# Kernel optimization log

Measured on AMD Instinct MI355X. Metric: run time of the kernel, lower is better.

Reference implementation:

```python
import jax, jax.numpy as jnp
import numpy as np
import math

NUM_HEADS = 16
N_WIRES = 8  # == d_k


def setup_inputs() -> dict:
    key = jax.random.key(0)
    k1, k2, k3, k4 = jax.random.split(key, 4)
    B, S, E = 4, 2048, NUM_HEADS * N_WIRES
    x = jax.random.normal(k1, (B, S, E), dtype=jnp.float32)
    theta = jax.random.normal(k2, (N_WIRES,), dtype=jnp.float32)
    W_combine = jax.random.normal(k3, (E, E), dtype=jnp.float32) * (1.0 / math.sqrt(E))
    b_combine = jax.random.normal(k4, (E,), dtype=jnp.float32) * 0.01
    return {"x": x, "theta": theta, "W_combine": W_combine, "b_combine": b_combine}


def _quantum_heads(x, theta, H, dk):
    # since single-qubit RX gates compose and the state stays a product state.
    B, S, E = x.shape
    proj = x.reshape(B, S, H, dk)  # [B,S,H,dk]
    return jnp.cos(proj + theta)   # theta broadcasts over wires (dk == n_wires)


def reference(x, theta, W_combine, b_combine):
    B, S, E = x.shape
    H, dk = NUM_HEADS, N_WIRES
    qkv = _quantum_heads(x, theta, H, dk)          # [B,S,H,dk]; q = k = v
    qh = jnp.transpose(qkv, (0, 2, 1, 3))           # [B,H,S,dk]
    scores = jnp.einsum('bhqd,bhkd->bhqk', qh, qh) / math.sqrt(dk)
    attn = jax.nn.softmax(scores, axis=-1)          # [B,H,S,S]
    out = jnp.einsum('bhqk,bhkd->bhqd', attn, qh)   # [B,H,S,dk]
    out = jnp.transpose(out, (0, 2, 1, 3)).reshape(B, S, E)
    return out @ W_combine.T + b_combine
```

## Files before the change

kernel.cpp:

```cpp
#include <hip/hip_runtime.h>

typedef _Float16 f16;
typedef _Float16 f16x2 __attribute__((ext_vector_type(2)));
typedef __fp16   h16x2 __attribute__((ext_vector_type(2)));
typedef _Float16 f16x4 __attribute__((ext_vector_type(4)));
typedef float    f32x4 __attribute__((ext_vector_type(4)));
typedef unsigned int u32;
typedef unsigned int u32x2v __attribute__((ext_vector_type(2)));

#define NB 4
#define NS 2048
#define NH 16
#define NDK 8
#define NE 128
#define CSCALE 0.51006972f

__device__ __forceinline__ float fexp2(float v){
#if __has_builtin(__builtin_amdgcn_exp2f)
  return __builtin_amdgcn_exp2f(v);
#else
  return exp2f(v);
#endif
}

__device__ __forceinline__ f16x2 pkrtz(float a, float b){
  return __builtin_bit_cast(f16x2, __builtin_amdgcn_cvt_pkrtz(a, b));
}

__device__ __forceinline__ float fdot2a(f16x2 a, f16x2 b, float c){
#if __has_builtin(__builtin_amdgcn_fdot2)
  return __builtin_amdgcn_fdot2(a, b, c, false);
#else
  return c + (float)a[0]*(float)b[0] + (float)a[1]*(float)b[1];
#endif
}

__global__ __launch_bounds__(256, 2) void qattn(const float* __restrict__ x,
                                                const float* __restrict__ theta,
                                                float* __restrict__ out){
  __shared__ __align__(16) uint2 Kl[NS*2];
  __shared__ __align__(16) uint2 Vl[8*512];

  const int bid = blockIdx.x;
  const int bh  = bid >> 3;
  const int qc  = bid & 7;
  const int b   = bh >> 4;
  const int h   = bh & 15;
  const int tid = threadIdx.x;

  const float4 th0 = *(const float4*)(theta);
  const float4 th1 = *(const float4*)(theta + 4);

  const float* xb = x + ((size_t)b*NS*NH + h)*NDK;
  unsigned short* Vs = (unsigned short*)Vl;
  #pragma unroll
  for(int i=0;i<8;++i){
    int s = tid + 256*i;
    const float4* xp = (const float4*)(xb + (size_t)s*(NH*NDK));
    float4 x0 = xp[0], x1 = xp[1];
    union { f16 hh[8]; uint4 u; } pk;
    pk.hh[0] = (f16)__cosf(x0.x + th0.x);
    pk.hh[1] = (f16)__cosf(x0.y + th0.y);
    pk.hh[2] = (f16)__cosf(x0.z + th0.z);
    pk.hh[3] = (f16)__cosf(x0.w + th0.w);
    pk.hh[4] = (f16)__cosf(x1.x + th1.x);
    pk.hh[5] = (f16)__cosf(x1.y + th1.y);
    pk.hh[6] = (f16)__cosf(x1.z + th1.z);
    pk.hh[7] = (f16)__cosf(x1.w + th1.w);
    ((uint4*)Kl)[s] = pk.u;
    int sb = s >> 2, sl = s & 3;
    #pragma unroll
    for(int d=0;d<8;++d)
      Vs[(d<<11) + (((sb ^ d)<<2) | sl)] =
          __builtin_bit_cast(unsigned short, pk.hh[d]);
  }
  __syncthreads();

  const int lane = tid & 63;
  const int w    = tid >> 6;
  const int c    = lane & 15;
  const int grp  = lane >> 4;
  const int g1   = grp & 1;
  const bool lo32  = (lane < 32);
  const bool creal = (c < 8);
  const int dvx  = c & 7;
  const int qbase = qc*256 + w*64;

  f16x4 qf[4];
  #pragma unroll
  for(int sub=0; sub<4; ++sub){
    uint2 qv = Kl[(qbase + sub*16 + c)*2 + g1];
    if(!lo32){ qv.x = 0u; qv.y = 0u; }
    qf[sub] = __builtin_bit_cast(f16x4, qv);
  }

  const f32x4 z4 = {0.f,0.f,0.f,0.f};
  f32x4 acc[4] = {z4,z4,z4,z4};
  uint2 ones2; ones2.x = 0x3C003C00u; ones2.y = 0x3C003C00u;

  const uint2* kptr = &Kl[c*2 + g1];
  for(int kt=0; kt<128; ++kt){
    uint2 ka = kptr[kt*32];
    uint2 va = Vl[(dvx<<9) | (((kt<<2) + grp) ^ dvx)];
    if(!creal) va = ones2;
    f16x4 kf = __builtin_bit_cast(f16x4, ka);
    f16x4 vf = __builtin_bit_cast(f16x4, va);
    #pragma unroll
    for(int sub=0; sub<4; ++sub){
      f32x4 st = __builtin_amdgcn_mfma_f32_16x16x16f16(kf, qf[sub], z4, 0, 0, 0);
      float p0 = fexp2(st[0]*CSCALE);
      float p1 = fexp2(st[1]*CSCALE);
      float p2 = fexp2(st[2]*CSCALE);
      float p3 = fexp2(st[3]*CSCALE);
      f16x2 plo = pkrtz(p0, p1);
      f16x2 phi = pkrtz(p2, p3);
      u32x2v pu = { __builtin_bit_cast(u32, plo), __builtin_bit_cast(u32, phi) };
      f16x4 pf = __builtin_bit_cast(f16x4, pu);
      acc[sub] = __builtin_amdgcn_mfma_f32_16x16x16f16(vf, pf, acc[sub], 0, 0, 0);
    }
  }

  #pragma unroll
  for(int sub=0; sub<4; ++sub){
    float den = __shfl(acc[sub][0], 32 + c, 64);
    if(lo32){
      float inv = 1.0f / den;
      int q = qbase + sub*16 + c;
      float4 o;
      o.x = acc[sub][0]*inv;
      o.y = acc[sub][1]*inv;
      o.z = acc[sub][2]*inv;
      o.w = acc[sub][3]*inv;
      *(float4*)(out + ((size_t)(b*NS + q)*NH + h)*NDK + grp*4) = o;
    }
  }
}

__global__ __launch_bounds__(256) void qcomb(const float* __restrict__ W,
                                             const float* __restrict__ bias,
                                             float* __restrict__ io){
  __shared__ __align__(16) u32 Wt[64*132];
  __shared__ __align__(16) u32 A2[32*65];
  const int tid = threadIdx.x;
  const size_t row0 = (size_t)blockIdx.x * 32;

  #pragma unroll
  for(int i=0;i<32;++i){
    int g = tid + 256*i;
    int j = g >> 6, e2 = g & 63;
    const float* wp = W + (size_t)j*NE + 2*e2;
    f16x2 wv = pkrtz(wp[0], wp[1]);
    Wt[e2*132 + j] = __builtin_bit_cast(u32, wv);
  }
  #pragma unroll
  for(int i=0;i<8;++i){
    int g = tid + 256*i;
    int r = g >> 6, e2 = g & 63;
    const float* ap = io + (row0 + r)*NE + 2*e2;
    f16x2 av = pkrtz(ap[0], ap[1]);
    A2[r*65 + e2] = __builtin_bit_cast(u32, av);
  }
  __syncthreads();

  const int tr = tid >> 4, tc = tid & 15;
  float acc0[8] = {0,0,0,0,0,0,0,0};
  float acc1[8] = {0,0,0,0,0,0,0,0};
  for(int e2=0; e2<64; ++e2){
    f16x2 a0 = __builtin_bit_cast(f16x2, A2[tr*65 + e2]);
    f16x2 a1 = __builtin_bit_cast(f16x2, A2[(tr+16)*65 + e2]);
    const u32* wr = &Wt[e2*132 + tc*8];
    #pragma unroll
    for(int cj=0; cj<8; ++cj){
      f16x2 wv = __builtin_bit_cast(f16x2, wr[cj]);
      acc0[cj] = fdot2a(a0, wv, acc0[cj]);
      acc1[cj] = fdot2a(a1, wv, acc1[cj]);
    }
  }

  float4 b0 = *(const float4*)(bias + tc*8);
  float4 b1 = *(const float4*)(bias + tc*8 + 4);
  float* o0 = io + (row0 + tr)*NE + tc*8;
  float* o1 = io + (row0 + tr + 16)*NE + tc*8;
  float4 v;
  v.x = acc0[0]+b0.x; v.y = acc0[1]+b0.y; v.z = acc0[2]+b0.z; v.w = acc0[3]+b0.w;
  *(float4*)(o0) = v;
  v.x = acc0[4]+b1.x; v.y = acc0[5]+b1.y; v.z = acc0[6]+b1.z; v.w = acc0[7]+b1.w;
  *(float4*)(o0+4) = v;
  v.x = acc1[0]+b0.x; v.y = acc1[1]+b0.y; v.z = acc1[2]+b0.z; v.w = acc1[3]+b0.w;
  *(float4*)(o1) = v;
  v.x = acc1[4]+b1.x; v.y = acc1[5]+b1.y; v.z = acc1[6]+b1.z; v.w = acc1[7]+b1.w;
  *(float4*)(o1+4) = v;
}

extern "C" void kernel_launch(void* const* d_in, const int* in_sizes, int n_in,
                              void* d_out, int out_size, void* d_ws, size_t ws_size,
                              hipStream_t stream) {
  (void)in_sizes; (void)n_in; (void)out_size; (void)d_ws; (void)ws_size;
  const float* x     = (const float*)d_in[0];
  const float* theta = (const float*)d_in[1];
  const float* W     = (const float*)d_in[2];
  const float* bias  = (const float*)d_in[3];
  float* out = (float*)d_out;

  qattn<<<512, 256, 0, stream>>>(x, theta, out);
  qcomb<<<256, 256, 0, stream>>>(W, bias, out);
}
```

Baseline: 57.05 us.

## Stream K/V in 512-key chunks with one query tile per wave

```diff
diff --git a/kernel.cpp b/kernel.cpp
--- a/kernel.cpp
+++ b/kernel.cpp
@@ -2,17 +2,17 @@
 
 typedef _Float16 f16;
 typedef _Float16 f16x2 __attribute__((ext_vector_type(2)));
-typedef __fp16   h16x2 __attribute__((ext_vector_type(2)));
 typedef _Float16 f16x4 __attribute__((ext_vector_type(4)));
 typedef float    f32x4 __attribute__((ext_vector_type(4)));
 typedef unsigned int u32;
 typedef unsigned int u32x2v __attribute__((ext_vector_type(2)));
 
-#define NB 4
 #define NS 2048
 #define NH 16
 #define NDK 8
 #define NE 128
+#define CHUNK 512
+#define NCHUNK 4
 #define CSCALE 0.51006972f
 
 __device__ __forceinline__ float fexp2(float v){
@@ -35,104 +35,124 @@
 #endif
 }
 
-__global__ __launch_bounds__(256, 2) void qattn(const float* __restrict__ x,
+__global__ __launch_bounds__(512, 8) void qattn(const float* __restrict__ x,
                                                 const float* __restrict__ theta,
                                                 float* __restrict__ out){
-  __shared__ __align__(16) uint2 Kl[NS*2];
-  __shared__ __align__(16) uint2 Vl[8*512];
-
-  const int bid = blockIdx.x;
-  const int bh  = bid >> 3;
-  const int qc  = bid & 7;
-  const int b   = bh >> 4;
-  const int h   = bh & 15;
-  const int tid = threadIdx.x;
-
-  const float4 th0 = *(const float4*)(theta);
-  const float4 th1 = *(const float4*)(theta + 4);
-
-  const float* xb = x + ((size_t)b*NS*NH + h)*NDK;
-  unsigned short* Vs = (unsigned short*)Vl;
-  #pragma unroll
-  for(int i=0;i<8;++i){
-    int s = tid + 256*i;
-    const float4* xp = (const float4*)(xb + (size_t)s*(NH*NDK));
-    float4 x0 = xp[0], x1 = xp[1];
-    union { f16 hh[8]; uint4 u; } pk;
-    pk.hh[0] = (f16)__cosf(x0.x + th0.x);
-    pk.hh[1] = (f16)__cosf(x0.y + th0.y);
-    pk.hh[2] = (f16)__cosf(x0.z + th0.z);
-    pk.hh[3] = (f16)__cosf(x0.w + th0.w);
-    pk.hh[4] = (f16)__cosf(x1.x + th1.x);
-    pk.hh[5] = (f16)__cosf(x1.y + th1.y);
-    pk.hh[6] = (f16)__cosf(x1.z + th1.z);
-    pk.hh[7] = (f16)__cosf(x1.w + th1.w);
-    ((uint4*)Kl)[s] = pk.u;
-    int sb = s >> 2, sl = s & 3;
-    #pragma unroll
-    for(int d=0;d<8;++d)
-      Vs[(d<<11) + (((sb ^ d)<<2) | sl)] =
-          __builtin_bit_cast(unsigned short, pk.hh[d]);
-  }
-  __syncthreads();
-
+  __shared__ __align__(16) uint4 Kc[CHUNK];
+  __shared__ __align__(16) unsigned short Vc[8*CHUNK];
+  __shared__ __align__(16) uint2 Ones[128];
+
+  const int bid  = blockIdx.x;
+  const int bh   = bid >> 4;
+  const int qc   = bid & 15;
+  const int b    = bh >> 4;
+  const int h    = bh & 15;
+  const int tid  = threadIdx.x;
   const int lane = tid & 63;
   const int w    = tid >> 6;
   const int c    = lane & 15;
   const int grp  = lane >> 4;
   const int g1   = grp & 1;
-  const bool lo32  = (lane < 32);
-  const bool creal = (c < 8);
+  const bool lo32 = lane < 32;
   const int dvx  = c & 7;
-  const int qbase = qc*256 + w*64;
-
-  f16x4 qf[4];
-  #pragma unroll
-  for(int sub=0; sub<4; ++sub){
-    uint2 qv = Kl[(qbase + sub*16 + c)*2 + g1];
-    if(!lo32){ qv.x = 0u; qv.y = 0u; }
-    qf[sub] = __builtin_bit_cast(f16x4, qv);
-  }
+
+  const float* xbh = x + (size_t)(b*NS*NH + h)*NDK;
+
+  if(tid < 64){
+    uint4 o; o.x = o.y = o.z = o.w = 0x3C003C00u;
+    ((uint4*)Ones)[tid] = o;
+  }
+
+  const int qrow = qc*128 + w*16 + c;
+  const float4 th4 = ((const float4*)theta)[g1];
+  const float4 xq = *(const float4*)(xbh + (size_t)qrow*(NH*NDK) + g1*4);
+  f16x2 qa = pkrtz(__cosf(xq.x+th4.x)*CSCALE, __cosf(xq.y+th4.y)*CSCALE);
+  f16x2 qb = pkrtz(__cosf(xq.z+th4.z)*CSCALE, __cosf(xq.w+th4.w)*CSCALE);
+  u32x2v qu = { lo32 ? __builtin_bit_cast(u32, qa) : 0u,
+                lo32 ? __builtin_bit_cast(u32, qb) : 0u };
+  const f16x4 qf = __builtin_bit_cast(f16x4, qu);
+
+  const uint2* kp  = (const uint2*)Kc + c*2 + g1;
+  const uint2* vp0 = (c < 8) ? ((const uint2*)Vc + dvx*128 + ((grp  ) ^ dvx))
+                             : Ones;
+  const uint2* vp1 = (c < 8) ? ((const uint2*)Vc + dvx*128 + ((4+grp) ^ dvx))
+                             : Ones;
+
+  const float4 thA = ((const float4*)theta)[0];
+  const float4 thB = ((const float4*)theta)[1];
 
   const f32x4 z4 = {0.f,0.f,0.f,0.f};
-  f32x4 acc[4] = {z4,z4,z4,z4};
-  uint2 ones2; ones2.x = 0x3C003C00u; ones2.y = 0x3C003C00u;
-
-  const uint2* kptr = &Kl[c*2 + g1];
-  for(int kt=0; kt<128; ++kt){
-    uint2 ka = kptr[kt*32];
-    uint2 va = Vl[(dvx<<9) | (((kt<<2) + grp) ^ dvx)];
-    if(!creal) va = ones2;
-    f16x4 kf = __builtin_bit_cast(f16x4, ka);
-    f16x4 vf = __builtin_bit_cast(f16x4, va);
+  f32x4 acc0 = z4, acc1 = z4;
+
+  float4 rx0 = *(const float4*)(xbh + (size_t)tid*(NH*NDK));
+  float4 rx1 = *(const float4*)(xbh + (size_t)tid*(NH*NDK) + 4);
+
+  for(int cc = 0; cc < NCHUNK; ++cc){
+    union { f16 hh[8]; uint4 u; } pk;
+    pk.hh[0] = (f16)__cosf(rx0.x + thA.x);
+    pk.hh[1] = (f16)__cosf(rx0.y + thA.y);
+    pk.hh[2] = (f16)__cosf(rx0.z + thA.z);
+    pk.hh[3] = (f16)__cosf(rx0.w + thA.w);
+    pk.hh[4] = (f16)__cosf(rx1.x + thB.x);
+    pk.hh[5] = (f16)__cosf(rx1.y + thB.y);
+    pk.hh[6] = (f16)__cosf(rx1.z + thB.z);
+    pk.hh[7] = (f16)__cosf(rx1.w + thB.w);
+    Kc[tid] = pk.u;
+    {
+      int sb = tid >> 2, sl = tid & 3;
+      #pragma unroll
+      for(int d = 0; d < 8; ++d)
+        Vc[d*CHUNK + (((sb ^ d) << 2) | sl)] =
+            __builtin_bit_cast(unsigned short, pk.hh[d]);
+    }
+    __syncthreads();
+
+    if(cc + 1 < NCHUNK){
+      const float* nx = xbh + (size_t)((cc+1)*CHUNK + tid)*(NH*NDK);
+      rx0 = *(const float4*)(nx);
+      rx1 = *(const float4*)(nx + 4);
+    }
+
     #pragma unroll
-    for(int sub=0; sub<4; ++sub){
-      f32x4 st = __builtin_amdgcn_mfma_f32_16x16x16f16(kf, qf[sub], z4, 0, 0, 0);
-      float p0 = fexp2(st[0]*CSCALE);
-      float p1 = fexp2(st[1]*CSCALE);
-      float p2 = fexp2(st[2]*CSCALE);
-      float p3 = fexp2(st[3]*CSCALE);
-      f16x2 plo = pkrtz(p0, p1);
-      f16x2 phi = pkrtz(p2, p3);
-      u32x2v pu = { __builtin_bit_cast(u32, plo), __builtin_bit_cast(u32, phi) };
-      f16x4 pf = __builtin_bit_cast(f16x4, pu);
-      acc[sub] = __builtin_amdgcn_mfma_f32_16x16x16f16(vf, pf, acc[sub], 0, 0, 0);
-    }
-  }
-
-  #pragma unroll
-  for(int sub=0; sub<4; ++sub){
-    float den = __shfl(acc[sub][0], 32 + c, 64);
-    if(lo32){
-      float inv = 1.0f / den;
-      int q = qbase + sub*16 + c;
-      float4 o;
-      o.x = acc[sub][0]*inv;
-      o.y = acc[sub][1]*inv;
-      o.z = acc[sub][2]*inv;
-      o.w = acc[sub][3]*inv;
-      *(float4*)(out + ((size_t)(b*NS + q)*NH + h)*NDK + grp*4) = o;
-    }
+    for(int m = 0; m < 16; ++m){
+      {
+        uint2 ka = kp[(2*m+0)*32];
+        uint2 va = vp0[m*8];
+        f16x4 kf = __builtin_bit_cast(f16x4, ka);
+        f16x4 vf = __builtin_bit_cast(f16x4, va);
+        f32x4 st = __builtin_amdgcn_mfma_f32_16x16x16f16(kf, qf, z4, 0, 0, 0);
+        f16x2 plo = pkrtz(fexp2(st[0]), fexp2(st[1]));
+        f16x2 phi = pkrtz(fexp2(st[2]), fexp2(st[3]));
+        u32x2v pu = { __builtin_bit_cast(u32, plo), __builtin_bit_cast(u32, phi) };
+        f16x4 pf = __builtin_bit_cast(f16x4, pu);
+        acc0 = __builtin_amdgcn_mfma_f32_16x16x16f16(vf, pf, acc0, 0, 0, 0);
+      }
+      {
+        uint2 ka = kp[(2*m+1)*32];
+        uint2 va = vp1[m*8];
+        f16x4 kf = __builtin_bit_cast(f16x4, ka);
+        f16x4 vf = __builtin_bit_cast(f16x4, va);
+        f32x4 st = __builtin_amdgcn_mfma_f32_16x16x16f16(kf, qf, z4, 0, 0, 0);
+        f16x2 plo = pkrtz(fexp2(st[0]), fexp2(st[1]));
+        f16x2 phi = pkrtz(fexp2(st[2]), fexp2(st[3]));
+        u32x2v pu = { __builtin_bit_cast(u32, plo), __builtin_bit_cast(u32, phi) };
+        f16x4 pf = __builtin_bit_cast(f16x4, pu);
+        acc1 = __builtin_amdgcn_mfma_f32_16x16x16f16(vf, pf, acc1, 0, 0, 0);
+      }
+    }
+
+    if(cc + 1 < NCHUNK) __syncthreads();
+  }
+
+  f32x4 accT;
+  accT[0] = acc0[0]+acc1[0]; accT[1] = acc0[1]+acc1[1];
+  accT[2] = acc0[2]+acc1[2]; accT[3] = acc0[3]+acc1[3];
+  float den = __shfl(accT[0], 32 + c, 64);
+  if(lo32){
+    float inv = 1.0f / den;
+    float4 o;
+    o.x = accT[0]*inv; o.y = accT[1]*inv; o.z = accT[2]*inv; o.w = accT[3]*inv;
+    *(float4*)(out + ((size_t)(b*NS + qrow)*NH + h)*NDK + grp*4) = o;
   }
 }
 
@@ -202,6 +222,6 @@
   const float* bias  = (const float*)d_in[3];
   float* out = (float*)d_out;
 
-  qattn<<<512, 256, 0, stream>>>(x, theta, out);
+  qattn<<<1024, 512, 0, stream>>>(x, theta, out);
   qcomb<<<256, 256, 0, stream>>>(W, bias, out);
 }
```

Result: faster. 49.50 us (-13.2%).
